# Optimization experiments

Measured on AMD Instinct MI355X. Metric: run time of the kernel, lower is better.

Reference implementation:

```python
import jax, jax.numpy as jnp
import numpy as np

N = 50000
F = 128
HID = 64
HEADS = 2
E = 800000
NEG = 0.2          # leaky_relu slope (GATConv default and decoder/attention)
BN_EPS = 1e-5


def setup_inputs() -> dict:
    key = jax.random.key(0)
    ks = jax.random.split(key, 24)
    s = 0.1
    inp = {
        "x": jax.random.normal(ks[0], (N, F), dtype=jnp.float32),
        "industry_edge_index": jax.random.randint(ks[1], (2, E), 0, N, dtype=jnp.int64),
        "universe_edge_index": jax.random.randint(ks[2], (2, E), 0, N, dtype=jnp.int64),
        # BatchNorm1d affine params
        "bn_gamma": jnp.ones((F,), jnp.float32),
        "bn_beta": jnp.zeros((F,), jnp.float32),
        # encoder: Linear(F, 2*HID) -> ReLU -> Linear(2*HID, HID) -> ReLU
        "enc_w1": jax.random.normal(ks[3], (F, 2 * HID), jnp.float32) * s,
        "enc_b1": jnp.zeros((2 * HID,), jnp.float32),
        "enc_w2": jax.random.normal(ks[4], (2 * HID, HID), jnp.float32) * s,
        "enc_b2": jnp.zeros((HID,), jnp.float32),
        # GATConv industry: lin weight [HID, HEADS*HID], att_src/att_dst [HEADS, HID], bias [HID]
        "gi_w": jax.random.normal(ks[5], (HID, HEADS * HID), jnp.float32) * s,
        "gi_att_src": jax.random.normal(ks[6], (HEADS, HID), jnp.float32) * s,
        "gi_att_dst": jax.random.normal(ks[7], (HEADS, HID), jnp.float32) * s,
        "gi_b": jnp.zeros((HID,), jnp.float32),
        # GATConv universe
        "gu_w": jax.random.normal(ks[8], (HID, HEADS * HID), jnp.float32) * s,
        "gu_att_src": jax.random.normal(ks[9], (HEADS, HID), jnp.float32) * s,
        "gu_att_dst": jax.random.normal(ks[10], (HEADS, HID), jnp.float32) * s,
        "gu_b": jnp.zeros((HID,), jnp.float32),
        # decoder: Linear(3*HID, HID) -> LeakyReLU(0.2) -> Linear(HID, 1)
        "dec_w1": jax.random.normal(ks[11], (3 * HID, HID), jnp.float32) * s,
        "dec_b1": jnp.zeros((HID,), jnp.float32),
        "dec_w2": jax.random.normal(ks[12], (HID, 1), jnp.float32) * s,
        "dec_b2": jnp.zeros((1,), jnp.float32),
        # factor attention: Linear(F, F)
        "fa_w": jax.random.normal(ks[13], (F, F), jnp.float32) * s,
        "fa_b": jnp.zeros((F,), jnp.float32),
    }
    return inp


def gat_conv(x, edge_index, W, att_src, att_dst, bias):
    """PyG GATConv, concat=False, add_self_loops=True, negative_slope=0.2."""
    n = x.shape[0]
    H, C = att_src.shape
    xl = (x @ W).reshape(n, H, C)                       # [N,H,C]
    loops = jnp.arange(n, dtype=edge_index.dtype)
    src = jnp.concatenate([edge_index[0], loops])       # [E+N]
    dst = jnp.concatenate([edge_index[1], loops])
    a_src = jnp.sum(xl * att_src, axis=-1)              # [N,H]
    a_dst = jnp.sum(xl * att_dst, axis=-1)
    e = jax.nn.leaky_relu(a_src[src] + a_dst[dst], NEG)  # [E+N,H]
    # scatter-softmax over incoming edges of each dst node
    emax = jax.ops.segment_max(jax.lax.stop_gradient(e), dst, num_segments=n)
    ee = jnp.exp(e - emax[dst])
    denom = jax.ops.segment_sum(ee, dst, num_segments=n)
    alpha = ee / denom[dst]                              # [E+N,H]
    msg = xl[src] * alpha[..., None]                     # [E+N,H,C]
    out = jax.ops.segment_sum(msg, dst, num_segments=n)  # [N,H,C]
    return out.mean(axis=1) + bias                       # concat=False -> head mean


def reference(x, industry_edge_index, universe_edge_index,
              bn_gamma, bn_beta, enc_w1, enc_b1, enc_w2, enc_b2,
              gi_w, gi_att_src, gi_att_dst, gi_b,
              gu_w, gu_att_src, gu_att_dst, gu_b,
              dec_w1, dec_b1, dec_w2, dec_b2, fa_w, fa_b):
    # BatchNorm1d (training mode: batch statistics)
    mean = jnp.mean(x, axis=0)
    var = jnp.var(x, axis=0)
    x_norm = (x - mean) / jnp.sqrt(var + BN_EPS) * bn_gamma + bn_beta
    # encoder
    h = jax.nn.relu(x_norm @ enc_w1 + enc_b1)
    Cenc = jax.nn.relu(h @ enc_w2 + enc_b2)              # [N,HID]
    # industry GAT + neutralization
    H_I = jax.nn.elu(gat_conv(Cenc, industry_edge_index, gi_w, gi_att_src, gi_att_dst, gi_b))
    C_I = Cenc - H_I
    # universe GAT + neutralization
    H_U = jax.nn.elu(gat_conv(C_I, universe_edge_index, gu_w, gu_att_src, gu_att_dst, gu_b))
    C_U = C_I - H_U
    hf = jnp.concatenate([Cenc, C_I, C_U], axis=-1)      # [N,3*HID]
    h2 = jax.nn.leaky_relu(hf @ dec_w1 + dec_b1, NEG)
    deep_factor = h2 @ dec_w2 + dec_b2                   # [N,1]
    U = jax.nn.leaky_relu(x @ fa_w + fa_b, NEG)
    attn_weights = jax.nn.softmax(U, axis=-1)            # [N,F]
    return deep_factor, attn_weights
```

## Files before the change

kernel.cpp:

```cpp
#include <hip/hip_runtime.h>
#include <hip/hip_bf16.h>
#include <math.h>

#define NNODES 50000
#define FDIM   128
#define HIDDIM 64
#define NEDGES 800000
#define NBLK64 782
#define N2     (2*NNODES)
#define NB_A   256
#define CHUNK  6250
#define NBUCK  391
#define NBPAD  512

__device__ __forceinline__ float leakyf(float x) { return x > 0.f ? x : 0.2f * x; }
__device__ __forceinline__ float eluf(float x)   { return x > 0.f ? x : expm1f(x); }

#define FMA8(A, xv, wa, wb) \
    A[0] += xv * wa.x; A[1] += xv * wa.y; A[2] += xv * wa.z; A[3] += xv * wa.w; \
    A[4] += xv * wb.x; A[5] += xv * wb.y; A[6] += xv * wb.z; A[7] += xv * wb.w;

__global__ void k_bn_stats(const float* __restrict__ x, float* __restrict__ acc, int n) {
    int t = threadIdx.x;
    int f = t & 127, half = t >> 7;
    int rows_per_block = (n + gridDim.x - 1) / gridDim.x;
    int r0 = blockIdx.x * rows_per_block;
    int r1 = min(r0 + rows_per_block, n);
    float s = 0.f, s2 = 0.f;
    for (int r = r0 + half; r < r1; r += 2) {
        float v = x[(size_t)r * 128 + f];
        s += v; s2 += v * v;
    }
    __shared__ float ls[256], ls2[256];
    ls[t] = s; ls2[t] = s2;
    __syncthreads();
    if (t < 128) {
        s  = ls[t]  + ls[t + 128];
        s2 = ls2[t] + ls2[t + 128];
        atomicAdd(&acc[f], s);
        atomicAdd(&acc[128 + f], s2);
    }
}

__global__ void k_bn_final(const float* __restrict__ acc, const float* __restrict__ gamma,
                           const float* __restrict__ beta, float* __restrict__ ss, int n) {
    int f = threadIdx.x;
    if (f < 128) {
        float inv_n = 1.0f / (float)n;
        float mean = acc[f] * inv_n;
        float var  = acc[128 + f] * inv_n - mean * mean;
        float sc = gamma[f] * rsqrtf(var + 1e-5f);
        ss[f] = sc;
        ss[128 + f] = beta[f] - mean * sc;
    }
}

__launch_bounds__(256, 4)
__global__ void k_encoder(const float* __restrict__ x, const float* __restrict__ bnss,
                          const float* __restrict__ w1, const float* __restrict__ b1,
                          const float* __restrict__ w2, const float* __restrict__ b2,
                          float* __restrict__ Cenc, int n_nodes) {
    __shared__ float Xs[64][133];
    int t = threadIdx.x;
    int r0 = blockIdx.x * 64;
#pragma unroll
    for (int it = 0; it < 8; ++it) {
        int idx = it * 256 + t;
        int row = idx >> 5;
        int col = (idx & 31) * 4;
        float4 v = make_float4(0.f, 0.f, 0.f, 0.f);
        if (r0 + row < n_nodes) v = *(const float4*)(x + (size_t)(r0 + row) * 128 + col);
        float4 sc = *(const float4*)(bnss + col);
        float4 sh = *(const float4*)(bnss + 128 + col);
        Xs[row][col + 0] = v.x * sc.x + sh.x;
        Xs[row][col + 1] = v.y * sc.y + sh.y;
        Xs[row][col + 2] = v.z * sc.z + sh.z;
        Xs[row][col + 3] = v.w * sc.w + sh.w;
    }
    __syncthreads();
    int cg = t & 15, rsub = t >> 4;
    int c0 = cg * 8, rbase = rsub * 4;
    float acc[4][8];
    {
        float4 ba = *(const float4*)(b1 + c0);
        float4 bb = *(const float4*)(b1 + c0 + 4);
#pragma unroll
        for (int j = 0; j < 4; ++j) {
            acc[j][0] = ba.x; acc[j][1] = ba.y; acc[j][2] = ba.z; acc[j][3] = ba.w;
            acc[j][4] = bb.x; acc[j][5] = bb.y; acc[j][6] = bb.z; acc[j][7] = bb.w;
        }
    }
    {
        float4 wA[4], wB[4];
#pragma unroll
        for (int d = 0; d < 4; ++d) {
            wA[d] = *(const float4*)(w1 + d * 128 + c0);
            wB[d] = *(const float4*)(w1 + d * 128 + c0 + 4);
        }
        for (int k = 0; k < 128; k += 4) {
#pragma unroll
            for (int d = 0; d < 4; ++d) {
                int kn = (k + 4 + d) & 127;
                float4 na = *(const float4*)(w1 + kn * 128 + c0);
                float4 nb = *(const float4*)(w1 + kn * 128 + c0 + 4);
                float x0 = Xs[rbase + 0][k + d];
                float x1 = Xs[rbase + 1][k + d];
                float x2 = Xs[rbase + 2][k + d];
                float x3 = Xs[rbase + 3][k + d];
                FMA8(acc[0], x0, wA[d], wB[d])
                FMA8(acc[1], x1, wA[d], wB[d])
                FMA8(acc[2], x2, wA[d], wB[d])
                FMA8(acc[3], x3, wA[d], wB[d])
                wA[d] = na; wB[d] = nb;
            }
        }
    }
    __syncthreads();
#pragma unroll
    for (int j = 0; j < 4; ++j)
#pragma unroll
        for (int i = 0; i < 8; ++i)
            Xs[rbase + j][c0 + i] = fmaxf(acc[j][i], 0.f);
    __syncthreads();
    int cg2 = t & 7, rs2 = t >> 3;
    int c2 = cg2 * 8, r2 = rs2 * 2;
    float a2[2][8];
    {
        float4 ba = *(const float4*)(b2 + c2);
        float4 bb = *(const float4*)(b2 + c2 + 4);
#pragma unroll
        for (int j = 0; j < 2; ++j) {
            a2[j][0] = ba.x; a2[j][1] = ba.y; a2[j][2] = ba.z; a2[j][3] = ba.w;
            a2[j][4] = bb.x; a2[j][5] = bb.y; a2[j][6] = bb.z; a2[j][7] = bb.w;
        }
    }
    {
        float4 wA[4], wB[4];
#pragma unroll
        for (int d = 0; d < 4; ++d) {
            wA[d] = *(const float4*)(w2 + d * 64 + c2);
            wB[d] = *(const float4*)(w2 + d * 64 + c2 + 4);
        }
        for (int k = 0; k < 128; k += 4) {
#pragma unroll
            for (int d = 0; d < 4; ++d) {
                int kn = (k + 4 + d) & 127;
                float4 na = *(const float4*)(w2 + kn * 64 + c2);
                float4 nb = *(const float4*)(w2 + kn * 64 + c2 + 4);
                float h0 = Xs[r2 + 0][k + d];
                float h1 = Xs[r2 + 1][k + d];
                FMA8(a2[0], h0, wA[d], wB[d])
                FMA8(a2[1], h1, wA[d], wB[d])
                wA[d] = na; wB[d] = nb;
            }
        }
    }
#pragma unroll
    for (int j = 0; j < 2; ++j) {
        int row = r0 + r2 + j;
        if (row < n_nodes) {
            float* o = Cenc + (size_t)row * 64 + c2;
            *(float4*)o       = make_float4(fmaxf(a2[j][0], 0.f), fmaxf(a2[j][1], 0.f),
                                            fmaxf(a2[j][2], 0.f), fmaxf(a2[j][3], 0.f));
            *(float4*)(o + 4) = make_float4(fmaxf(a2[j][4], 0.f), fmaxf(a2[j][5], 0.f),
                                            fmaxf(a2[j][6], 0.f), fmaxf(a2[j][7], 0.f));
        }
    }
}

__launch_bounds__(256, 4)
__global__ void k_xl(const float* __restrict__ Cin, const float* __restrict__ Wg,
                     const float* __restrict__ attS, const float* __restrict__ attD,
                     float* __restrict__ xl, float* __restrict__ asrc, float* __restrict__ adst,
                     int n_nodes) {
    __shared__ float Cs[64][65];
    int t = threadIdx.x;
    int r0 = blockIdx.x * 64;
#pragma unroll
    for (int it = 0; it < 4; ++it) {
        int idx = it * 256 + t;
        int row = idx >> 4;
        int col = (idx & 15) * 4;
        float4 v = make_float4(0.f, 0.f, 0.f, 0.f);
        if (r0 + row < n_nodes) v = *(const float4*)(Cin + (size_t)(r0 + row) * 64 + col);
        Cs[row][col + 0] = v.x; Cs[row][col + 1] = v.y;
        Cs[row][col + 2] = v.z; Cs[row][col + 3] = v.w;
    }
    __syncthreads();
    int cg = t & 15, rsub = t >> 4;
    int c0 = cg * 8, rbase = rsub * 4;
    float acc[4][8];
#pragma unroll
    for (int j = 0; j < 4; ++j)
#pragma unroll
        for (int i = 0; i < 8; ++i) acc[j][i] = 0.f;
    {
        float4 wA[4], wB[4];
#pragma unroll
        for (int d = 0; d < 4; ++d) {
            wA[d] = *(const float4*)(Wg + d * 128 + c0);
            wB[d] = *(const float4*)(Wg + d * 128 + c0 + 4);
        }
        for (int k = 0; k < 64; k += 4) {
#pragma unroll
            for (int d = 0; d < 4; ++d) {
                int kn = (k + 4 + d) & 63;
                float4 na = *(const float4*)(Wg + kn * 128 + c0);
                float4 nb = *(const float4*)(Wg + kn * 128 + c0 + 4);
                float x0 = Cs[rbase + 0][k + d];
                float x1 = Cs[rbase + 1][k + d];
                float x2 = Cs[rbase + 2][k + d];
                float x3 = Cs[rbase + 3][k + d];
                FMA8(acc[0], x0, wA[d], wB[d])
                FMA8(acc[1], x1, wA[d], wB[d])
                FMA8(acc[2], x2, wA[d], wB[d])
                FMA8(acc[3], x3, wA[d], wB[d])
                wA[d] = na; wB[d] = nb;
            }
        }
    }
#pragma unroll
    for (int j = 0; j < 4; ++j) {
        int row = r0 + rbase + j;
        if (row < n_nodes) {
            float* o = xl + (size_t)row * 128 + c0;
            *(float4*)o       = make_float4(acc[j][0], acc[j][1], acc[j][2], acc[j][3]);
            *(float4*)(o + 4) = make_float4(acc[j][4], acc[j][5], acc[j][6], acc[j][7]);
        }
    }
    int head = cg >> 3;
    const float* as_ = attS + head * 64 + (cg & 7) * 8;
    const float* ad_ = attD + head * 64 + (cg & 7) * 8;
    float4 sa = *(const float4*)as_,       sb = *(const float4*)(as_ + 4);
    float4 da = *(const float4*)ad_,       db = *(const float4*)(ad_ + 4);
    float ps[4], pd[4];
#pragma unroll
    for (int j = 0; j < 4; ++j) {
        ps[j] = acc[j][0]*sa.x + acc[j][1]*sa.y + acc[j][2]*sa.z + acc[j][3]*sa.w
              + acc[j][4]*sb.x + acc[j][5]*sb.y + acc[j][6]*sb.z + acc[j][7]*sb.w;
        pd[j] = acc[j][0]*da.x + acc[j][1]*da.y + acc[j][2]*da.z + acc[j][3]*da.w
              + acc[j][4]*db.x + acc[j][5]*db.y + acc[j][6]*db.z + acc[j][7]*db.w;
#pragma unroll
        for (int off = 1; off < 8; off <<= 1) {
            ps[j] += __shfl_xor(ps[j], off, 64);
            pd[j] += __shfl_xor(pd[j], off, 64);
        }
    }
    if ((cg & 7) == 0) {
#pragma unroll
        for (int j = 0; j < 4; ++j) {
            int row = r0 + rbase + j;
            if (row < n_nodes) {
                asrc[2 * row + head] = ps[j];
                adst[2 * row + head] = pd[j];
            }
        }
    }
}

__launch_bounds__(256)
__global__ void k_hist(const int* __restrict__ ei_i, const int* __restrict__ ei_u,
                       int* __restrict__ counts) {
    __shared__ int hist[NBPAD];
    int t = threadIdx.x, blk = blockIdx.x;
    for (int i = t; i < NBPAD; i += 256) hist[i] = 0;
    __syncthreads();
    int p0 = blk * CHUNK;
    for (int k = 0; k < CHUNK; k += 256) {
        if (k + t < CHUNK) {
            int p = p0 + k + t;
            int d2 = (p < NEDGES) ? ei_i[NEDGES + p]
                                  : (NNODES + ei_u[NEDGES + (p - NEDGES)]);
            atomicAdd(&hist[d2 >> 8], 1);
        }
    }
    __syncthreads();
    for (int i = t; i < NBPAD; i += 256) counts[blk * NBPAD + i] = hist[i];
}

__launch_bounds__(256)
__global__ void k_rowscan(const int* __restrict__ counts, int* __restrict__ offsets,
                          int* __restrict__ totals) {
    __shared__ int sd[256];
    int b = blockIdx.x;
    int t = threadIdx.x;
    int v = counts[t * NBPAD + b];
    sd[t] = v;
    __syncthreads();
    for (int off = 1; off < 256; off <<= 1) {
        int u = (t >= off) ? sd[t - off] : 0;
        __syncthreads();
        sd[t] += u;
        __syncthreads();
    }
    offsets[t * NBPAD + b] = sd[t] - v;
    if (t == 255) totals[b] = sd[255];
}

__launch_bounds__(512)
__global__ void k_bscan(const int* __restrict__ totals, int* __restrict__ bucketBase) {
    __shared__ int sd[512];
    int t = threadIdx.x;
    int v = totals[t];
    sd[t] = v; __syncthreads();
    for (int off = 1; off < 512; off <<= 1) {
        int u = (t >= off) ? sd[t - off] : 0;
        __syncthreads();
        sd[t] += u;
        __syncthreads();
    }
    bucketBase[t] = sd[t] - v;
    if (t == 511) bucketBase[512] = sd[511];
}

__launch_bounds__(256, 2)
__global__ void k_stage(const int* __restrict__ ei_i, const int* __restrict__ ei_u,
                        const int* __restrict__ offsets, const int* __restrict__ bucketBase,
                        unsigned int* __restrict__ staging) {
    __shared__ int hist[NBPAD];
    __shared__ int runstart[NBPAD];
    __shared__ int cursor[NBPAD];
    __shared__ int delta[NBPAD];
    __shared__ int sd[256];
    __shared__ unsigned int sorted[CHUNK];
    __shared__ unsigned short slotb[CHUNK];
    int t = threadIdx.x, blk = blockIdx.x;
    for (int i = t; i < NBPAD; i += 256) hist[i] = 0;
    __syncthreads();
    int p0 = blk * CHUNK;
    for (int k = 0; k < CHUNK; k += 256) {
        if (k + t < CHUNK) {
            int p = p0 + k + t;
            int d2 = (p < NEDGES) ? ei_i[NEDGES + p]
                                  : (NNODES + ei_u[NEDGES + (p - NEDGES)]);
            atomicAdd(&hist[d2 >> 8], 1);
        }
    }
    __syncthreads();
    int v0 = hist[2 * t], v1 = hist[2 * t + 1];
    int s = v0 + v1;
    sd[t] = s; __syncthreads();
    for (int off = 1; off < 256; off <<= 1) {
        int u = (t >= off) ? sd[t - off] : 0;
        __syncthreads();
        sd[t] += u;
        __syncthreads();
    }
    int base = sd[t] - s;
    runstart[2 * t] = base;
    runstart[2 * t + 1] = base + v0;
    __syncthreads();
    for (int i = t; i < NBPAD; i += 256) {
        cursor[i] = runstart[i];
        delta[i] = bucketBase[i] + offsets[blk * NBPAD + i] - runstart[i];
    }
    __syncthreads();
    for (int k = 0; k < CHUNK; k += 256) {
        if (k + t < CHUNK) {
            int p = p0 + k + t;
            int src, d2;
            if (p < NEDGES) { src = ei_i[p]; d2 = ei_i[NEDGES + p]; }
            else { int q = p - NEDGES; src = ei_u[q]; d2 = NNODES + ei_u[NEDGES + q]; }
            int b = d2 >> 8;
            int pos = atomicAdd(&cursor[b], 1);
            sorted[pos] = ((unsigned)src << 8) | (unsigned)(d2 & 255);
            slotb[pos] = (unsigned short)b;
        }
    }
    __syncthreads();
    for (int k = t; k < CHUNK; k += 256) {
        int b = slotb[k];
        staging[delta[b] + k] = sorted[k];
    }
}

__launch_bounds__(256)
__global__ void k_binsort(const unsigned int* __restrict__ staging,
                          const int* __restrict__ bucketBase,
                          int* __restrict__ ssrc, int* __restrict__ offs2) {
    __shared__ int hist[256];
    __shared__ int cursor[256];
    __shared__ int sd[256];
    int b = blockIdx.x, t = threadIdx.x;
    int base = bucketBase[b];
    int cnt  = bucketBase[b + 1] - base;
    hist[t] = 0;
    __syncthreads();
    for (int p = t; p < cnt; p += 256)
        atomicAdd(&hist[staging[base + p] & 255u], 1);
    __syncthreads();
    int v = hist[t];
    sd[t] = v; __syncthreads();
    for (int off = 1; off < 256; off <<= 1) {
        int u = (t >= off) ? sd[t - off] : 0;
        __syncthreads();
        sd[t] += u;
        __syncthreads();
    }
    int excl = sd[t] - v;
    cursor[t] = excl;
    int d2 = b * 256 + t;
    if (d2 <= N2) offs2[d2] = base + excl;
    __syncthreads();
    for (int p = t; p < cnt; p += 256) {
        unsigned int e = staging[base + p];
        int pos = atomicAdd(&cursor[e & 255u], 1);
        ssrc[base + pos] = (int)(e >> 8);
    }
}

__launch_bounds__(256)
__global__ void k_gat_agg(const float* __restrict__ Cin, const float* __restrict__ xl,
                          const float* __restrict__ asrc, const float* __restrict__ adst,
                          const int* __restrict__ offs, const int* __restrict__ ssrc,
                          const float* __restrict__ bias, float* __restrict__ Cout,
                          int n_nodes) {
    int wid = (blockIdx.x * blockDim.x + threadIdx.x) >> 6;
    int lane = threadIdx.x & 63;
    if (wid >= n_nodes) return;
    int n = wid;
    int h = lane >> 5;
    int beg = offs[n], end = offs[n + 1];
    float adh = adst[2 * n + h];
    const float2* xl2 = (const float2*)xl;
    float ee = __expf(leakyf(asrc[2 * n + h] + adh));
    float2 v = xl2[(size_t)n * 64 + lane];
    float acc0 = ee * v.x, acc1 = ee * v.y, dn = ee;
    for (int i = beg; i < end; ++i) {
        int s = ssrc[i];
        float e2 = __expf(leakyf(asrc[2 * s + h] + adh));
        float2 u = xl2[(size_t)s * 64 + lane];
        acc0 += e2 * u.x; acc1 += e2 * u.y; dn += e2;
    }
    float inv = 1.0f / dn;
    float o0 = acc0 * inv, o1 = acc1 * inv;
    float p0 = __shfl_xor(o0, 32, 64);
    float p1 = __shfl_xor(o1, 32, 64);
    if (lane < 32) {
        int c0 = 2 * lane;
        float hv0 = eluf(0.5f * (o0 + p0) + bias[c0]);
        float hv1 = eluf(0.5f * (o1 + p1) + bias[c0 + 1]);
        float2 cv = *(const float2*)(Cin + (size_t)n * 64 + c0);
        *(float2*)(Cout + (size_t)n * 64 + c0) = make_float2(cv.x - hv0, cv.y - hv1);
    }
}

__launch_bounds__(256, 3)
__global__ void k_dec(const float* __restrict__ Cenc, const float* __restrict__ CI,
                      const float* __restrict__ CU, const float* __restrict__ w1,
                      const float* __restrict__ b1, const float* __restrict__ w2,
                      const float* __restrict__ b2, float* __restrict__ out, int n_nodes) {
    __shared__ float Fs[64][193];
    int t = threadIdx.x;
    int r0 = blockIdx.x * 64;
    const float* srcs[3] = {Cenc, CI, CU};
#pragma unroll
    for (int s = 0; s < 3; ++s) {
        const float* src = srcs[s];
#pragma unroll
        for (int it = 0; it < 4; ++it) {
            int idx = it * 256 + t;
            int row = idx >> 4;
            int col = (idx & 15) * 4;
            float4 v = make_float4(0.f, 0.f, 0.f, 0.f);
            if (r0 + row < n_nodes) v = *(const float4*)(src + (size_t)(r0 + row) * 64 + col);
            Fs[row][s * 64 + col + 0] = v.x; Fs[row][s * 64 + col + 1] = v.y;
            Fs[row][s * 64 + col + 2] = v.z; Fs[row][s * 64 + col + 3] = v.w;
        }
    }
    __syncthreads();
    int cg = t & 7, rs = t >> 3;
    int c0 = cg * 8, r2 = rs * 2;
    float acc[2][8];
    {
        float4 ba = *(const float4*)(b1 + c0);
        float4 bb = *(const float4*)(b1 + c0 + 4);
#pragma unroll
        for (int j = 0; j < 2; ++j) {
            acc[j][0] = ba.x; acc[j][1] = ba.y; acc[j][2] = ba.z; acc[j][3] = ba.w;
            acc[j][4] = bb.x; acc[j][5] = bb.y; acc[j][6] = bb.z; acc[j][7] = bb.w;
        }
    }
    {
        float4 wA[4], wB[4];
#pragma unroll
        for (int d = 0; d < 4; ++d) {
            wA[d] = *(const float4*)(w1 + d * 64 + c0);
            wB[d] = *(const float4*)(w1 + d * 64 + c0 + 4);
        }
        for (int k = 0; k < 192; k += 4) {
#pragma unroll
            for (int d = 0; d < 4; ++d) {
                int kn = k + 4 + d; if (kn > 191) kn = 191;
                float4 na = *(const float4*)(w1 + kn * 64 + c0);
                float4 nb = *(const float4*)(w1 + kn * 64 + c0 + 4);
                float f0 = Fs[r2 + 0][k + d];
                float f1 = Fs[r2 + 1][k + d];
                FMA8(acc[0], f0, wA[d], wB[d])
                FMA8(acc[1], f1, wA[d], wB[d])
                wA[d] = na; wB[d] = nb;
            }
        }
    }
    float4 w2a = *(const float4*)(w2 + c0);
    float4 w2b = *(const float4*)(w2 + c0 + 4);
    float b2v = b2[0];
#pragma unroll
    for (int j = 0; j < 2; ++j) {
        float p = leakyf(acc[j][0])*w2a.x + leakyf(acc[j][1])*w2a.y
                + leakyf(acc[j][2])*w2a.z + leakyf(acc[j][3])*w2a.w
                + leakyf(acc[j][4])*w2b.x + leakyf(acc[j][5])*w2b.y
                + leakyf(acc[j][6])*w2b.z + leakyf(acc[j][7])*w2b.w;
#pragma unroll
        for (int off = 1; off < 8; off <<= 1) p += __shfl_xor(p, off, 64);
        int row = r0 + r2 + j;
        if (cg == 0 && row < n_nodes) out[row] = p + b2v;
    }
}

__launch_bounds__(256, 4)
__global__ void k_fa(const float* __restrict__ x, const float* __restrict__ w,
                     const float* __restrict__ b, float* __restrict__ attn, int n_nodes) {
    __shared__ float Xs[64][133];
    int t = threadIdx.x;
    int r0 = blockIdx.x * 64;
#pragma unroll
    for (int it = 0; it < 8; ++it) {
        int idx = it * 256 + t;
        int row = idx >> 5;
        int col = (idx & 31) * 4;
        float4 v = make_float4(0.f, 0.f, 0.f, 0.f);
        if (r0 + row < n_nodes) v = *(const float4*)(x + (size_t)(r0 + row) * 128 + col);
        Xs[row][col + 0] = v.x; Xs[row][col + 1] = v.y;
        Xs[row][col + 2] = v.z; Xs[row][col + 3] = v.w;
    }
    __syncthreads();
    int cg = t & 15, rsub = t >> 4;
    int c0 = cg * 8, rbase = rsub * 4;
    float acc[4][8];
    {
        float4 ba = *(const float4*)(b + c0);
        float4 bb = *(const float4*)(b + c0 + 4);
#pragma unroll
        for (int j = 0; j < 4; ++j) {
            acc[j][0] = ba.x; acc[j][1] = ba.y; acc[j][2] = ba.z; acc[j][3] = ba.w;
            acc[j][4] = bb.x; acc[j][5] = bb.y; acc[j][6] = bb.z; acc[j][7] = bb.w;
        }
    }
    {
        float4 wA[4], wB[4];
#pragma unroll
        for (int d = 0; d < 4; ++d) {
            wA[d] = *(const float4*)(w + d * 128 + c0);
            wB[d] = *(const float4*)(w + d * 128 + c0 + 4);
        }
        for (int k = 0; k < 128; k += 4) {
#pragma unroll
            for (int d = 0; d < 4; ++d) {
                int kn = (k + 4 + d) & 127;
                float4 na = *(const float4*)(w + kn * 128 + c0);
                float4 nb = *(const float4*)(w + kn * 128 + c0 + 4);
                float x0 = Xs[rbase + 0][k + d];
                float x1 = Xs[rbase + 1][k + d];
                float x2 = Xs[rbase + 2][k + d];
                float x3 = Xs[rbase + 3][k + d];
                FMA8(acc[0], x0, wA[d], wB[d])
                FMA8(acc[1], x1, wA[d], wB[d])
                FMA8(acc[2], x2, wA[d], wB[d])
                FMA8(acc[3], x3, wA[d], wB[d])
                wA[d] = na; wB[d] = nb;
            }
        }
    }
#pragma unroll
    for (int j = 0; j < 4; ++j) {
        float m = -1e30f;
#pragma unroll
        for (int i = 0; i < 8; ++i) {
            acc[j][i] = leakyf(acc[j][i]);
            m = fmaxf(m, acc[j][i]);
        }
#pragma unroll
        for (int off = 1; off < 16; off <<= 1) m = fmaxf(m, __shfl_xor(m, off, 64));
        float s = 0.f;
#pragma unroll
        for (int i = 0; i < 8; ++i) {
            acc[j][i] = __expf(acc[j][i] - m);
            s += acc[j][i];
        }
#pragma unroll
        for (int off = 1; off < 16; off <<= 1) s += __shfl_xor(s, off, 64);
        float inv = 1.0f / s;
        int row = r0 + rbase + j;
        if (row < n_nodes) {
            float* o = attn + (size_t)row * 128 + c0;
            *(float4*)o       = make_float4(acc[j][0]*inv, acc[j][1]*inv, acc[j][2]*inv, acc[j][3]*inv);
            *(float4*)(o + 4) = make_float4(acc[j][4]*inv, acc[j][5]*inv, acc[j][6]*inv, acc[j][7]*inv);
        }
    }
}

extern "C" void kernel_launch(void* const* d_in, const int* in_sizes, int n_in,
                              void* d_out, int out_size, void* d_ws, size_t ws_size,
                              hipStream_t stream) {
    const float* x        = (const float*)d_in[0];
    const int*   ei_ind   = (const int*)d_in[1];
    const int*   ei_uni   = (const int*)d_in[2];
    const float* bn_gamma = (const float*)d_in[3];
    const float* bn_beta  = (const float*)d_in[4];
    const float* enc_w1   = (const float*)d_in[5];
    const float* enc_b1   = (const float*)d_in[6];
    const float* enc_w2   = (const float*)d_in[7];
    const float* enc_b2   = (const float*)d_in[8];
    const float* gi_w     = (const float*)d_in[9];
    const float* gi_as    = (const float*)d_in[10];
    const float* gi_ad    = (const float*)d_in[11];
    const float* gi_b     = (const float*)d_in[12];
    const float* gu_w     = (const float*)d_in[13];
    const float* gu_as    = (const float*)d_in[14];
    const float* gu_ad    = (const float*)d_in[15];
    const float* gu_b     = (const float*)d_in[16];
    const float* dec_w1   = (const float*)d_in[17];
    const float* dec_b1   = (const float*)d_in[18];
    const float* dec_w2   = (const float*)d_in[19];
    const float* dec_b2   = (const float*)d_in[20];
    const float* fa_w     = (const float*)d_in[21];
    const float* fa_b     = (const float*)d_in[22];

    const int N = NNODES, E = NEDGES;

    float* Cenc  = (float*)d_ws;
    float* C_I   = Cenc + (size_t)N * 64;
    float* C_U   = C_I + (size_t)N * 64;
    float* xl    = C_U + (size_t)N * 64;
    float* a_src = xl + (size_t)N * 128;
    float* a_dst = a_src + (size_t)N * 2;
    float* bnacc = a_dst + (size_t)N * 2;
    float* bnss  = bnacc + 256;
    int* offs2      = (int*)(bnss + 256);
    int* ssrc2      = offs2 + (N2 + 1);
    int* counts     = ssrc2 + 2 * E;
    int* offsets    = counts + NB_A * NBPAD;
    int* totals     = offsets + NB_A * NBPAD;
    int* bucketBase = totals + NBPAD;
    unsigned int* staging = (unsigned int*)xl;

    float* out_deep = (float*)d_out;
    float* out_attn = out_deep + N;

    hipMemsetAsync(bnacc, 0, 256 * sizeof(float), stream);
    k_bn_stats<<<256, 256, 0, stream>>>(x, bnacc, N);
    k_bn_final<<<1, 128, 0, stream>>>(bnacc, bn_gamma, bn_beta, bnss, N);

    k_encoder<<<NBLK64, 256, 0, stream>>>(x, bnss, enc_w1, enc_b1, enc_w2, enc_b2, Cenc, N);

    k_hist<<<NB_A, 256, 0, stream>>>(ei_ind, ei_uni, counts);
    k_rowscan<<<NBPAD, 256, 0, stream>>>(counts, offsets, totals);
    k_bscan<<<1, 512, 0, stream>>>(totals, bucketBase);
    k_stage<<<NB_A, 256, 0, stream>>>(ei_ind, ei_uni, offsets, bucketBase, staging);
    k_binsort<<<NBUCK, 256, 0, stream>>>(staging, bucketBase, ssrc2, offs2);

    k_xl<<<NBLK64, 256, 0, stream>>>(Cenc, gi_w, gi_as, gi_ad, xl, a_src, a_dst, N);
    k_gat_agg<<<(N + 3) / 4, 256, 0, stream>>>(Cenc, xl, a_src, a_dst, offs2, ssrc2, gi_b, C_I, N);

    k_xl<<<NBLK64, 256, 0, stream>>>(C_I, gu_w, gu_as, gu_ad, xl, a_src, a_dst, N);
    k_gat_agg<<<(N + 3) / 4, 256, 0, stream>>>(C_I, xl, a_src, a_dst, offs2 + N, ssrc2, gu_b, C_U, N);

    k_dec<<<NBLK64, 256, 0, stream>>>(Cenc, C_I, C_U, dec_w1, dec_b1, dec_w2, dec_b2, out_deep, N);
    k_fa<<<NBLK64, 256, 0, stream>>>(x, fa_w, fa_b, out_attn, N);
}
```

Before: 628.5 us.

## Store GAT projected features in fp16, reuse histogram counts, unroll aggregation

The per-node projected features xl are now written as fp16 by k_xl and read as half2 in k_gat_agg. This halves the bytes moved by the random-gather aggregation over about 1.6M edges. k_stage now reads per-block bucket counts from k_hist's output instead of recomputing the histogram, and the aggregation loop is unrolled by two so more gathers are in flight. The cost is reduced precision of the projected features, so results may drift slightly from the fp32 reference.

```diff
diff --git a/kernel.cpp b/kernel.cpp
--- a/kernel.cpp
+++ b/kernel.cpp
@@ -1,5 +1,6 @@
 #include <hip/hip_runtime.h>
 #include <hip/hip_bf16.h>
+#include <hip/hip_fp16.h>
 #include <math.h>
 
 #define NNODES 50000
@@ -171,7 +172,7 @@
 __launch_bounds__(256, 4)
 __global__ void k_xl(const float* __restrict__ Cin, const float* __restrict__ Wg,
                      const float* __restrict__ attS, const float* __restrict__ attD,
-                     float* __restrict__ xl, float* __restrict__ asrc, float* __restrict__ adst,
+                     __half* __restrict__ xl, float* __restrict__ asrc, float* __restrict__ adst,
                      int n_nodes) {
     __shared__ float Cs[64][65];
     int t = threadIdx.x;
@@ -223,9 +224,11 @@
     for (int j = 0; j < 4; ++j) {
         int row = r0 + rbase + j;
         if (row < n_nodes) {
-            float* o = xl + (size_t)row * 128 + c0;
-            *(float4*)o       = make_float4(acc[j][0], acc[j][1], acc[j][2], acc[j][3]);
-            *(float4*)(o + 4) = make_float4(acc[j][4], acc[j][5], acc[j][6], acc[j][7]);
+            __half2 h4[4];
+#pragma unroll
+            for (int q = 0; q < 4; ++q)
+                h4[q] = __float22half2_rn(make_float2(acc[j][2*q], acc[j][2*q+1]));
+            *(float4*)(xl + (size_t)row * 128 + c0) = *(float4*)h4;
         }
     }
     int head = cg >> 3;
@@ -315,9 +318,9 @@
 
 __launch_bounds__(256, 2)
 __global__ void k_stage(const int* __restrict__ ei_i, const int* __restrict__ ei_u,
+                        const int* __restrict__ counts,
                         const int* __restrict__ offsets, const int* __restrict__ bucketBase,
                         unsigned int* __restrict__ staging) {
-    __shared__ int hist[NBPAD];
     __shared__ int runstart[NBPAD];
     __shared__ int cursor[NBPAD];
     __shared__ int delta[NBPAD];
@@ -325,19 +328,8 @@
     __shared__ unsigned int sorted[CHUNK];
     __shared__ unsigned short slotb[CHUNK];
     int t = threadIdx.x, blk = blockIdx.x;
-    for (int i = t; i < NBPAD; i += 256) hist[i] = 0;
-    __syncthreads();
-    int p0 = blk * CHUNK;
-    for (int k = 0; k < CHUNK; k += 256) {
-        if (k + t < CHUNK) {
-            int p = p0 + k + t;
-            int d2 = (p < NEDGES) ? ei_i[NEDGES + p]
-                                  : (NNODES + ei_u[NEDGES + (p - NEDGES)]);
-            atomicAdd(&hist[d2 >> 8], 1);
-        }
-    }
-    __syncthreads();
-    int v0 = hist[2 * t], v1 = hist[2 * t + 1];
+    int v0 = counts[blk * NBPAD + 2 * t];
+    int v1 = counts[blk * NBPAD + 2 * t + 1];
     int s = v0 + v1;
     sd[t] = s; __syncthreads();
     for (int off = 1; off < 256; off <<= 1) {
@@ -355,6 +347,7 @@
         delta[i] = bucketBase[i] + offsets[blk * NBPAD + i] - runstart[i];
     }
     __syncthreads();
+    int p0 = blk * CHUNK;
     for (int k = 0; k < CHUNK; k += 256) {
         if (k + t < CHUNK) {
             int p = p0 + k + t;
@@ -410,7 +403,7 @@
 }
 
 __launch_bounds__(256)
-__global__ void k_gat_agg(const float* __restrict__ Cin, const float* __restrict__ xl,
+__global__ void k_gat_agg(const float* __restrict__ Cin, const __half* __restrict__ xl,
                           const float* __restrict__ asrc, const float* __restrict__ adst,
                           const int* __restrict__ offs, const int* __restrict__ ssrc,
                           const float* __restrict__ bias, float* __restrict__ Cout,
@@ -422,15 +415,29 @@
     int h = lane >> 5;
     int beg = offs[n], end = offs[n + 1];
     float adh = adst[2 * n + h];
-    const float2* xl2 = (const float2*)xl;
+    const __half2* xh = (const __half2*)xl;
     float ee = __expf(leakyf(asrc[2 * n + h] + adh));
-    float2 v = xl2[(size_t)n * 64 + lane];
+    float2 v = __half22float2(xh[(size_t)n * 64 + lane]);
     float acc0 = ee * v.x, acc1 = ee * v.y, dn = ee;
-    for (int i = beg; i < end; ++i) {
-        int s = ssrc[i];
-        float e2 = __expf(leakyf(asrc[2 * s + h] + adh));
-        float2 u = xl2[(size_t)s * 64 + lane];
-        acc0 += e2 * u.x; acc1 += e2 * u.y; dn += e2;
+    int i = beg;
+    for (; i + 1 < end; i += 2) {
+        int s0 = ssrc[i], s1 = ssrc[i + 1];
+        __half2 u0 = xh[(size_t)s0 * 64 + lane];
+        __half2 u1 = xh[(size_t)s1 * 64 + lane];
+        float e0 = __expf(leakyf(asrc[2 * s0 + h] + adh));
+        float e1 = __expf(leakyf(asrc[2 * s1 + h] + adh));
+        float2 f0 = __half22float2(u0);
+        float2 f1 = __half22float2(u1);
+        acc0 += e0 * f0.x + e1 * f1.x;
+        acc1 += e0 * f0.y + e1 * f1.y;
+        dn   += e0 + e1;
+    }
+    if (i < end) {
+        int s0 = ssrc[i];
+        __half2 u0 = xh[(size_t)s0 * 64 + lane];
+        float e0 = __expf(leakyf(asrc[2 * s0 + h] + adh));
+        float2 f0 = __half22float2(u0);
+        acc0 += e0 * f0.x; acc1 += e0 * f0.y; dn += e0;
     }
     float inv = 1.0f / dn;
     float o0 = acc0 * inv, o1 = acc1 * inv;
@@ -632,8 +639,8 @@
     float* Cenc  = (float*)d_ws;
     float* C_I   = Cenc + (size_t)N * 64;
     float* C_U   = C_I + (size_t)N * 64;
-    float* xl    = C_U + (size_t)N * 64;
-    float* a_src = xl + (size_t)N * 128;
+    float* xlf   = C_U + (size_t)N * 64;
+    float* a_src = xlf + (size_t)N * 128;
     float* a_dst = a_src + (size_t)N * 2;
     float* bnacc = a_dst + (size_t)N * 2;
     float* bnss  = bnacc + 256;
@@ -643,7 +650,8 @@
     int* offsets    = counts + NB_A * NBPAD;
     int* totals     = offsets + NB_A * NBPAD;
     int* bucketBase = totals + NBPAD;
-    unsigned int* staging = (unsigned int*)xl;
+    __half* xl = (__half*)xlf;
+    unsigned int* staging = (unsigned int*)(xlf + (size_t)N * 64);
 
     float* out_deep = (float*)d_out;
     float* out_attn = out_deep + N;
@@ -657,7 +665,7 @@
     k_hist<<<NB_A, 256, 0, stream>>>(ei_ind, ei_uni, counts);
     k_rowscan<<<NBPAD, 256, 0, stream>>>(counts, offsets, totals);
     k_bscan<<<1, 512, 0, stream>>>(totals, bucketBase);
-    k_stage<<<NB_A, 256, 0, stream>>>(ei_ind, ei_uni, offsets, bucketBase, staging);
+    k_stage<<<NB_A, 256, 0, stream>>>(ei_ind, ei_uni, counts, offsets, bucketBase, staging);
     k_binsort<<<NBUCK, 256, 0, stream>>>(staging, bucketBase, ssrc2, offs2);
 
     k_xl<<<NBLK64, 256, 0, stream>>>(Cenc, gi_w, gi_as, gi_ad, xl, a_src, a_dst, N);
```

After: 541.7 us. 1.16x faster.
